# Kernel optimization log

Hardware: AMD Instinct MI355X
Metric: run time of the kernel (lower is better)

The kernel has to match this reference:

```python
import jax, jax.numpy as jnp
import numpy as np

L, D, HQ, HKV, HD, P, V, B, S = 4, 2048, 16, 4, 128, 8192, 32000, 2, 1024
THETA, EPS = 500000.0, 1e-5
RATIO = HQ // HKV  # GQA q-to-kv ratio = 4


def rmsnorm(x, w):
    # torch: w * (x * rsqrt(mean(x^2, -1) + eps)) computed in fp32
    x32 = x.astype(jnp.float32)
    n = x32 * jax.lax.rsqrt(jnp.mean(x32 * x32, axis=-1, keepdims=True) + EPS)
    return w * n.astype(x.dtype)


def make_rope(seq_len):
    inv = 1.0 / (THETA ** (jnp.arange(0, HD, 2, dtype=jnp.float32) / HD))  # [HD/2]
    ang = jnp.arange(seq_len, dtype=jnp.float32)[:, None] * inv[None, :]   # [S, HD/2]
    return jnp.cos(ang)[None, :, None, :], jnp.sin(ang)[None, :, None, :]  # [1,S,1,HD/2]


def rope(t, cos, sin):
    # torch code: complex = t[..., :HD/2] + i*t[..., HD/2:], multiply by e^{i*ang},
    # then view_as_real + flatten -> INTERLEAVED (r0,i0,r1,i1,...) output layout.
    h = HD // 2
    r, im = t[..., :h], t[..., h:]
    orr = r * cos - im * sin
    oim = r * sin + im * cos
    return jnp.stack([orr, oim], axis=-1).reshape(t.shape)


def attention(x, wqkv, wo, cos, sin):
    b, s, _ = x.shape
    qkv = x @ wqkv                               # [b,s,D+2*HKV*HD]
    q = qkv[..., :D].reshape(b, s, HQ, HD)
    k = qkv[..., D:D + HKV * HD].reshape(b, s, HKV, HD)
    v = qkv[..., D + HKV * HD:].reshape(b, s, HKV, HD)
    q = rope(q, cos, sin)
    k = rope(k, cos, sin)
    # GQA: repeat_interleave kv heads to match q heads (offset=0 prefill; cache is identity)
    k = jnp.repeat(k, RATIO, axis=2)
    v = jnp.repeat(v, RATIO, axis=2)
    scale = 1.0 / np.sqrt(HD)
    scores = jnp.einsum('bqhd,bkhd->bhqk', q, k) * scale
    causal = jnp.tril(jnp.ones((s, s), dtype=bool))
    scores = jnp.where(causal[None, None], scores, jnp.finfo(scores.dtype).min)
    probs = jax.nn.softmax(scores, axis=-1)
    out = jnp.einsum('bhqk,bkhd->bqhd', probs, v).reshape(b, s, D)
    return out @ wo


def swiglu(x, wgu, wd):
    gu = x @ wgu                                  # [b,s,2P]
    gate, up = gu[..., :P], gu[..., P:]
    return (jax.nn.silu(gate) * up) @ wd


def setup_inputs() -> dict:
    key = jax.random.key(0)
    ks = jax.random.split(key, 8)
    sc = 0.02
    return {
        'tokens': jax.random.randint(ks[0], (B, S), 0, V),
        'emb': jax.random.normal(ks[1], (V, D), jnp.float32) * sc,
        'w_qkv': jax.random.normal(ks[2], (L, D, D + 2 * HKV * HD), jnp.float32) * sc,
        'w_o': jax.random.normal(ks[3], (L, D, D), jnp.float32) * sc,
        'w_gate_up': jax.random.normal(ks[4], (L, D, 2 * P), jnp.float32) * sc,
        'w_down': jax.random.normal(ks[5], (L, P, D), jnp.float32) * sc,
        'ln_attn': jnp.ones((L, D), jnp.float32),
        'ln_ffn': jnp.ones((L, D), jnp.float32),
        'ln_f': jnp.ones((D,), jnp.float32),
        'w_lm': jax.random.normal(ks[6], (D, V), jnp.float32) * sc,
    }


def reference(tokens, emb, w_qkv, w_o, w_gate_up, w_down, ln_attn, ln_ffn, ln_f, w_lm):
    cos, sin = make_rope(S)
    x = emb[tokens]                               # [B,S,D]
    for l in range(L):
        x = x + attention(rmsnorm(x, ln_attn[l]), w_qkv[l], w_o[l], cos, sin)
        x = x + swiglu(rmsnorm(x, ln_ffn[l]), w_gate_up[l], w_down[l])
    return rmsnorm(x, ln_f) @ w_lm                # logits [B,S,V]
```

## Files before the change

kernel.cpp:

```cpp
#include <hip/hip_runtime.h>
#include <hip/hip_bf16.h>
#include <math.h>

#define S_LEN 1024
#define DIM   2048
#define NHQ   16
#define NHKV  4
#define HDIM  128
#define PDIM  8192
#define VOCAB 32000
#define NLAYER 4
#define NROWS (2 * S_LEN)

typedef __attribute__((ext_vector_type(4))) float f32x4;
typedef __attribute__((ext_vector_type(8))) short bf16x8;

__device__ __forceinline__ void gload_lds16(const void* g, void* l) {
  __builtin_amdgcn_global_load_lds(
      (const __attribute__((address_space(1))) unsigned int*)g,
      (__attribute__((address_space(3))) unsigned int*)l, 16, 0, 0);
}

#define FENCE() asm volatile("" ::: "memory")

__global__ __launch_bounds__(256) void k_embed(const int* __restrict__ tokens,
    const float* __restrict__ emb, float* __restrict__ x) {
  int row = blockIdx.x;
  int tok = tokens[row];
  const f32x4* src = (const f32x4*)(emb + (size_t)tok * DIM);
  f32x4* dst = (f32x4*)(x + (size_t)row * DIM);
  for (int i = threadIdx.x; i < DIM / 4; i += 256) dst[i] = src[i];
}

__global__ __launch_bounds__(256) void k_rmsnorm(const float* __restrict__ x,
    const float* __restrict__ w, __hip_bfloat16* __restrict__ out) {
  int row = blockIdx.x;
  const float* xr = x + (size_t)row * DIM;
  float ss = 0.f;
  for (int i = threadIdx.x; i < DIM; i += 256) { float v = xr[i]; ss += v * v; }
  for (int off = 32; off; off >>= 1) ss += __shfl_xor(ss, off);
  __shared__ float wsum[4];
  if ((threadIdx.x & 63) == 0) wsum[threadIdx.x >> 6] = ss;
  __syncthreads();
  float tot = wsum[0] + wsum[1] + wsum[2] + wsum[3];
  float r = rsqrtf(tot / (float)DIM + 1e-5f);
  __hip_bfloat16* orow = out + (size_t)row * DIM;
  for (int i = threadIdx.x; i < DIM; i += 256)
    orow[i] = __float2bfloat16(w[i] * (xr[i] * r));
}

__global__ __launch_bounds__(256) void k_wt(const float* __restrict__ W,
    __hip_bfloat16* __restrict__ WT, int K, int N) {
  __shared__ __hip_bfloat16 t[64][72];
  int k0 = blockIdx.y * 64, n0 = blockIdx.x * 64;
  int r = threadIdx.x >> 4;
  int c4 = (threadIdx.x & 15) * 4;
#pragma unroll
  for (int i = 0; i < 4; ++i) {
    int k = r + i * 16;
    f32x4 v = *(const f32x4*)(W + (size_t)(k0 + k) * N + n0 + c4);
#pragma unroll
    for (int j = 0; j < 4; ++j) t[c4 + j][k] = __float2bfloat16(v[j]);
  }
  __syncthreads();
  int n = threadIdx.x >> 2, kc = (threadIdx.x & 3) * 16;
  bf16x8* dst = (bf16x8*)(WT + (size_t)(n0 + n) * K + k0 + kc);
  dst[0] = *(const bf16x8*)&t[n][kc];
  dst[1] = *(const bf16x8*)&t[n][kc + 8];
}

template<int EPI>
__global__ __launch_bounds__(512) void k_gemm256(
    const __hip_bfloat16* __restrict__ A, const __hip_bfloat16* __restrict__ BT,
    void* __restrict__ Cv, int M, int N, int K) {
  __shared__ __hip_bfloat16 As[2][256][64];
  __shared__ __hip_bfloat16 Bs[2][256][64];
  int tid = threadIdx.x;
  int bid = blockIdx.x;
  int mt = bid & 7, nt = bid >> 3;
  int bm = mt << 8, bn = nt << 8;
  int wave = tid >> 6, lane = tid & 63;
  int wm = wave >> 2, wn = wave & 3;
  int g = lane >> 4, c = lane & 15;
  f32x4 acc[8][4] = {};

  auto stage = [&](int buf, int k0) {
#pragma unroll
    for (int i = 0; i < 4; ++i) {
      int ci = i * 512 + tid;
      int row = ci >> 3, pc = ci & 7;
      int jl = pc ^ (row & 7);
      gload_lds16(A + (size_t)(bm + row) * K + k0 + jl * 8, &As[buf][row][pc * 8]);
      gload_lds16(BT + (size_t)(bn + row) * K + k0 + jl * 8, &Bs[buf][row][pc * 8]);
    }
  };

  int ntiles = K >> 6;
  stage(0, 0);
  if (ntiles > 1) stage(1, 64);

  for (int t = 0; t < ntiles; ++t) {
    int cur = t & 1;
    if (t + 1 < ntiles) asm volatile("s_waitcnt vmcnt(8)" ::: "memory");
    else                asm volatile("s_waitcnt vmcnt(0)" ::: "memory");
    __builtin_amdgcn_s_barrier();
    FENCE();
    __builtin_amdgcn_sched_barrier(0);
#pragma unroll
    for (int kk = 0; kk < 2; ++kk) {
      bf16x8 af[8], bv[4];
#pragma unroll
      for (int mi = 0; mi < 8; ++mi) {
        int row = wm * 128 + mi * 16 + c;
        int ch = (kk * 4 + g) ^ (row & 7);
        af[mi] = *(const bf16x8*)&As[cur][row][ch * 8];
      }
#pragma unroll
      for (int ni = 0; ni < 4; ++ni) {
        int row = wn * 64 + ni * 16 + c;
        int ch = (kk * 4 + g) ^ (row & 7);
        bv[ni] = *(const bf16x8*)&Bs[cur][row][ch * 8];
      }
      __builtin_amdgcn_s_setprio(1);
#pragma unroll
      for (int mi = 0; mi < 8; ++mi)
#pragma unroll
        for (int ni = 0; ni < 4; ++ni)
          acc[mi][ni] = __builtin_amdgcn_mfma_f32_16x16x32_bf16(af[mi], bv[ni], acc[mi][ni], 0, 0, 0);
      __builtin_amdgcn_s_setprio(0);
    }
    FENCE();
    __builtin_amdgcn_s_barrier();
    FENCE();
    if (t + 2 < ntiles) stage(cur, (t + 2) << 6);
  }

  float* Cf = (float*)Cv;
  __hip_bfloat16* Cb = (__hip_bfloat16*)Cv;
  int row0 = bm + wm * 128, col0 = bn + wn * 64;
#pragma unroll
  for (int mi = 0; mi < 8; ++mi)
#pragma unroll
    for (int ni = 0; ni < 4; ++ni)
#pragma unroll
      for (int r = 0; r < 4; ++r) {
        int row = row0 + mi * 16 + g * 4 + r;
        int col = col0 + ni * 16 + c;
        size_t idx = (size_t)row * N + col;
        if (EPI == 0) Cf[idx] = acc[mi][ni][r];
        else if (EPI == 1) Cf[idx] += acc[mi][ni][r];
        else Cb[idx] = __float2bfloat16(acc[mi][ni][r]);
      }
}

template<int EPI>
__global__ __launch_bounds__(256) void k_gemm_bt(
    const __hip_bfloat16* __restrict__ A, const __hip_bfloat16* __restrict__ BT,
    void* __restrict__ Cv, int M, int N, int K) {
  __shared__ __hip_bfloat16 As[2][128][64];
  __shared__ __hip_bfloat16 Bs[2][128][64];
  int nm = M >> 7;
  int bid = blockIdx.x;
  int mt, nt;
  if (nm == 16) {
    int xcd = bid & 7;
    int seq = bid >> 3;
    mt = (xcd << 1) | (seq & 1);
    nt = seq >> 1;
  } else {
    mt = bid % nm;
    nt = bid / nm;
  }
  int bm = mt << 7, bn = nt << 7;
  int tid  = threadIdx.x;
  int wave = tid >> 6, lane = tid & 63;
  int wr = (wave >> 1) * 64, wc = (wave & 1) * 64;
  int g = lane >> 4, c = lane & 15;
  f32x4 acc[4][4] = {};

  auto stage = [&](int buf, int k0) {
#pragma unroll
    for (int i = 0; i < 4; ++i) {
      int ci = i * 256 + tid;
      int row = ci >> 3, pc = ci & 7;
      int jl = pc ^ (row & 7);
      gload_lds16(A + (size_t)(bm + row) * K + k0 + jl * 8, &As[buf][row][pc * 8]);
      gload_lds16(BT + (size_t)(bn + row) * K + k0 + jl * 8, &Bs[buf][row][pc * 8]);
    }
  };

  int ntiles = K >> 6;
  stage(0, 0);
  if (ntiles > 1) stage(1, 64);

  for (int t = 0; t < ntiles; ++t) {
    int cur = t & 1;
    if (t + 1 < ntiles) asm volatile("s_waitcnt vmcnt(8)" ::: "memory");
    else                asm volatile("s_waitcnt vmcnt(0)" ::: "memory");
    __builtin_amdgcn_s_barrier();
    FENCE();
    __builtin_amdgcn_sched_barrier(0);
#pragma unroll
    for (int kk = 0; kk < 2; ++kk) {
      bf16x8 af[4], bv[4];
#pragma unroll
      for (int mi = 0; mi < 4; ++mi) {
        int row = wr + mi * 16 + c;
        int ch = (kk * 4 + g) ^ (row & 7);
        af[mi] = *(const bf16x8*)&As[cur][row][ch * 8];
      }
#pragma unroll
      for (int ni = 0; ni < 4; ++ni) {
        int row = wc + ni * 16 + c;
        int ch = (kk * 4 + g) ^ (row & 7);
        bv[ni] = *(const bf16x8*)&Bs[cur][row][ch * 8];
      }
      __builtin_amdgcn_s_setprio(1);
#pragma unroll
      for (int mi = 0; mi < 4; ++mi)
#pragma unroll
        for (int ni = 0; ni < 4; ++ni)
          acc[mi][ni] = __builtin_amdgcn_mfma_f32_16x16x32_bf16(af[mi], bv[ni], acc[mi][ni], 0, 0, 0);
      __builtin_amdgcn_s_setprio(0);
    }
    FENCE();
    __builtin_amdgcn_s_barrier();
    FENCE();
    if (t + 2 < ntiles) stage(cur, (t + 2) << 6);
  }

  float* Cf = (float*)Cv;
  __hip_bfloat16* Cb = (__hip_bfloat16*)Cv;
#pragma unroll
  for (int mi = 0; mi < 4; ++mi)
#pragma unroll
    for (int ni = 0; ni < 4; ++ni)
#pragma unroll
      for (int r = 0; r < 4; ++r) {
        int row = bm + wr + mi * 16 + g * 4 + r;
        int col = bn + wc + ni * 16 + c;
        size_t idx = (size_t)row * N + col;
        if (EPI == 0) Cf[idx] = acc[mi][ni][r];
        else if (EPI == 1) Cf[idx] += acc[mi][ni][r];
        else Cb[idx] = __float2bfloat16(acc[mi][ni][r]);
      }
}

template<int EPI>
__global__ __launch_bounds__(256) void k_gemm(
    const __hip_bfloat16* __restrict__ A, const float* __restrict__ Bw,
    void* __restrict__ Cv, int M, int N, int K) {
  __shared__ __hip_bfloat16 As[128][32];
  __shared__ __hip_bfloat16 Bs[128][40];
  int tid  = threadIdx.x;
  int bm = blockIdx.y * 128, bn = blockIdx.x * 128;
  int wave = tid >> 6, lane = tid & 63;
  int wr = (wave >> 1) * 64, wc = (wave & 1) * 64;
  int lrow = lane & 15, lk = (lane >> 4) * 8;
  f32x4 acc[4][4] = {};
  for (int k0 = 0; k0 < K; k0 += 32) {
#pragma unroll
    for (int i = 0; i < 2; ++i) {
      int L = i * 256 + tid;
      int row = L >> 2, koff = (L & 3) * 8;
      gload_lds16(A + (size_t)(bm + row) * K + k0 + koff, &As[row][koff]);
    }
#pragma unroll
    for (int i = 0; i < 4; ++i) {
      int L = i * 256 + tid;
      int kk = L >> 5;
      int c4 = (L & 31) * 4;
      f32x4 v = *(const f32x4*)(Bw + (size_t)(k0 + kk) * N + bn + c4);
#pragma unroll
      for (int j = 0; j < 4; ++j) Bs[c4 + j][kk] = __float2bfloat16(v[j]);
    }
    __syncthreads();
    bf16x8 af[4], bfr[4];
#pragma unroll
    for (int mi = 0; mi < 4; ++mi)
      af[mi] = *(const bf16x8*)(&As[wr + mi * 16 + lrow][lk]);
#pragma unroll
    for (int ni = 0; ni < 4; ++ni)
      bfr[ni] = *(const bf16x8*)(&Bs[wc + ni * 16 + lrow][lk]);
#pragma unroll
    for (int mi = 0; mi < 4; ++mi)
#pragma unroll
      for (int ni = 0; ni < 4; ++ni)
        acc[mi][ni] = __builtin_amdgcn_mfma_f32_16x16x32_bf16(af[mi], bfr[ni], acc[mi][ni], 0, 0, 0);
    __syncthreads();
  }
  float* Cf = (float*)Cv;
  __hip_bfloat16* Cb = (__hip_bfloat16*)Cv;
#pragma unroll
  for (int mi = 0; mi < 4; ++mi)
#pragma unroll
    for (int ni = 0; ni < 4; ++ni)
#pragma unroll
      for (int r = 0; r < 4; ++r) {
        int row = bm + wr + mi * 16 + ((lane >> 4) * 4 + r);
        int col = bn + wc + ni * 16 + (lane & 15);
        size_t idx = (size_t)row * N + col;
        if (EPI == 0) Cf[idx] = acc[mi][ni][r];
        else if (EPI == 1) Cf[idx] += acc[mi][ni][r];
        else Cb[idx] = __float2bfloat16(acc[mi][ni][r]);
      }
}

__global__ __launch_bounds__(256) void k_rope(const float* __restrict__ qkv,
    __hip_bfloat16* __restrict__ qr, __hip_bfloat16* __restrict__ kr,
    __hip_bfloat16* __restrict__ vt) {
  int rowid = blockIdx.x;
  int b = rowid >> 10, s = rowid & (S_LEN - 1);
  const float* src = qkv + (size_t)rowid * 3072;
  const float kInvLog = 0.20503692777f;
  const float scale = 0.08838834764831845f;
  __shared__ float cs[64], sn[64];
  if (threadIdx.x < 64) {
    float inv = expf(-(float)threadIdx.x * kInvLog);
    float a = (float)s * inv;
    sincosf(a, &sn[threadIdx.x], &cs[threadIdx.x]);
  }
  __syncthreads();
  for (int it = threadIdx.x; it < NHQ * 64; it += 256) {
    int h = it >> 6, i = it & 63;
    float re = src[h * HDIM + i], im = src[h * HDIM + 64 + i];
    size_t dst = ((size_t)(b * NHQ + h) * S_LEN + s) * HDIM;
    qr[dst + 2 * i]     = __float2bfloat16((re * cs[i] - im * sn[i]) * scale);
    qr[dst + 2 * i + 1] = __float2bfloat16((re * sn[i] + im * cs[i]) * scale);
  }
  for (int it = threadIdx.x; it < NHKV * 64; it += 256) {
    int h = it >> 6, i = it & 63;
    float re = src[DIM + h * HDIM + i], im = src[DIM + h * HDIM + 64 + i];
    size_t dst = ((size_t)(b * NHKV + h) * S_LEN + s) * HDIM;
    kr[dst + 2 * i]     = __float2bfloat16(re * cs[i] - im * sn[i]);
    kr[dst + 2 * i + 1] = __float2bfloat16(re * sn[i] + im * cs[i]);
  }
  for (int it = threadIdx.x; it < NHKV * HDIM; it += 256) {
    int h = it >> 7, d = it & 127;
    vt[(((size_t)b * NHKV + h) * HDIM + d) * S_LEN + s] =
        __float2bfloat16(src[DIM + NHKV * HDIM + it]);
  }
}

__global__ __launch_bounds__(256) void k_attn_mfma(
    const __hip_bfloat16* __restrict__ Q,
    const __hip_bfloat16* __restrict__ Kc,
    const __hip_bfloat16* __restrict__ VT,
    __hip_bfloat16* __restrict__ O) {
  __shared__ __hip_bfloat16 plds[4][16][40];
  int wave = threadIdx.x >> 6, lane = threadIdx.x & 63;
  int gw = blockIdx.x * 4 + wave;
  int qt = gw & 63;
  int bh = gw >> 6;
  int b = bh >> 4, h = bh & 15;
  int hk = h >> 2;
  int q0 = qt * 16;
  int g = lane >> 4, c = lane & 15;
  const __hip_bfloat16* Qb = Q + ((size_t)bh * S_LEN + q0) * HDIM;
  const __hip_bfloat16* Kb = Kc + (size_t)(b * NHKV + hk) * S_LEN * HDIM;
  const __hip_bfloat16* Vb = VT + (size_t)(b * NHKV + hk) * S_LEN * HDIM;

  bf16x8 qf[4];
#pragma unroll
  for (int cn = 0; cn < 4; ++cn)
    qf[cn] = *(const bf16x8*)(Qb + (size_t)c * HDIM + cn * 32 + g * 8);

  f32x4 po[8] = {};
  float m[4], l[4];
#pragma unroll
  for (int r = 0; r < 4; ++r) { m[r] = -1e30f; l[r] = 0.f; }

  int kvend = q0 + 16;
  for (int kv0 = 0; kv0 < kvend; kv0 += 32) {
    f32x4 s0 = {}, s1 = {};
#pragma unroll
    for (int cn = 0; cn < 4; ++cn) {
      bf16x8 k0f = *(const bf16x8*)(Kb + (size_t)(kv0 + c) * HDIM + cn * 32 + g * 8);
      bf16x8 k1f = *(const bf16x8*)(Kb + (size_t)(kv0 + 16 + c) * HDIM + cn * 32 + g * 8);
      s0 = __builtin_amdgcn_mfma_f32_16x16x32_bf16(qf[cn], k0f, s0, 0, 0, 0);
      s1 = __builtin_amdgcn_mfma_f32_16x16x32_bf16(qf[cn], k1f, s1, 0, 0, 0);
    }
    if (kv0 + 31 > q0) {
#pragma unroll
      for (int r = 0; r < 4; ++r) {
        int qrow = q0 + g * 4 + r;
        if (kv0 + c > qrow)      s0[r] = -1e30f;
        if (kv0 + 16 + c > qrow) s1[r] = -1e30f;
      }
    }
    float rm[4];
#pragma unroll
    for (int r = 0; r < 4; ++r) rm[r] = fmaxf(s0[r], s1[r]);
#pragma unroll
    for (int off = 1; off < 16; off <<= 1)
#pragma unroll
      for (int r = 0; r < 4; ++r) rm[r] = fmaxf(rm[r], __shfl_xor(rm[r], off));
    float p0[4], p1[4], rs[4];
#pragma unroll
    for (int r = 0; r < 4; ++r) {
      float mn = fmaxf(m[r], rm[r]);
      float corr = __expf(m[r] - mn);
      m[r] = mn;
      p0[r] = __expf(s0[r] - mn);
      p1[r] = __expf(s1[r] - mn);
      rs[r] = p0[r] + p1[r];
      l[r] *= corr;
#pragma unroll
      for (int t = 0; t < 8; ++t) po[t][r] *= corr;
    }
#pragma unroll
    for (int off = 1; off < 16; off <<= 1)
#pragma unroll
      for (int r = 0; r < 4; ++r) rs[r] += __shfl_xor(rs[r], off);
#pragma unroll
    for (int r = 0; r < 4; ++r) l[r] += rs[r];
#pragma unroll
    for (int r = 0; r < 4; ++r) {
      plds[wave][g * 4 + r][c]      = __float2bfloat16(p0[r]);
      plds[wave][g * 4 + r][16 + c] = __float2bfloat16(p1[r]);
    }
    bf16x8 pf = *(const bf16x8*)&plds[wave][c][g * 8];
#pragma unroll
    for (int t = 0; t < 8; ++t) {
      bf16x8 vf = *(const bf16x8*)(Vb + (size_t)(t * 16 + c) * S_LEN + kv0 + g * 8);
      po[t] = __builtin_amdgcn_mfma_f32_16x16x32_bf16(pf, vf, po[t], 0, 0, 0);
    }
  }
  float inv[4];
#pragma unroll
  for (int r = 0; r < 4; ++r) inv[r] = 1.f / l[r];
  __hip_bfloat16* ob = O + ((size_t)(b * S_LEN) + q0) * DIM + h * HDIM;
#pragma unroll
  for (int t = 0; t < 8; ++t)
#pragma unroll
    for (int r = 0; r < 4; ++r)
      ob[(size_t)(g * 4 + r) * DIM + t * 16 + c] = __float2bfloat16(po[t][r] * inv[r]);
}

__global__ __launch_bounds__(256) void k_swiglu(const __hip_bfloat16* __restrict__ gu,
    __hip_bfloat16* __restrict__ h) {
  size_t i = (size_t)blockIdx.x * 256 + threadIdx.x;
  size_t row = i >> 10, c8 = (i & 1023) * 8;
  const __hip_bfloat16* grow = gu + row * (2 * PDIM);
  bf16x8 gv = *(const bf16x8*)(grow + c8);
  bf16x8 uv = *(const bf16x8*)(grow + PDIM + c8);
  const __hip_bfloat16* gp = (const __hip_bfloat16*)&gv;
  const __hip_bfloat16* up = (const __hip_bfloat16*)&uv;
  __hip_bfloat16 ov[8];
#pragma unroll
  for (int j = 0; j < 8; ++j) {
    float g = __bfloat162float(gp[j]);
    float u = __bfloat162float(up[j]);
    float s = g / (1.f + __expf(-g));
    ov[j] = __float2bfloat16(s * u);
  }
  *(bf16x8*)(h + row * PDIM + c8) = *(const bf16x8*)ov;
}

extern "C" void kernel_launch(void* const* d_in, const int* in_sizes, int n_in,
                              void* d_out, int out_size, void* d_ws, size_t ws_size,
                              hipStream_t stream) {
  const int*   tokens    = (const int*)d_in[0];
  const float* emb       = (const float*)d_in[1];
  const float* w_qkv     = (const float*)d_in[2];
  const float* w_o       = (const float*)d_in[3];
  const float* w_gate_up = (const float*)d_in[4];
  const float* w_down    = (const float*)d_in[5];
  const float* ln_attn   = (const float*)d_in[6];
  const float* ln_ffn    = (const float*)d_in[7];
  const float* ln_f      = (const float*)d_in[8];
  const float* w_lm      = (const float*)d_in[9];
  float* out = (float*)d_out;

  char* ws = (char*)d_ws;
  float* x = (float*)ws;                    ws += (size_t)NROWS * DIM * 4;
  __hip_bfloat16* xn = (__hip_bfloat16*)ws; ws += (size_t)NROWS * DIM * 2;
  float* qkv = (float*)ws;                  ws += (size_t)NROWS * 3072 * 4;
  __hip_bfloat16* qr = (__hip_bfloat16*)ws; ws += (size_t)2 * NHQ * S_LEN * HDIM * 2;
  __hip_bfloat16* kr = (__hip_bfloat16*)ws; ws += (size_t)2 * NHKV * S_LEN * HDIM * 2;
  __hip_bfloat16* vt = (__hip_bfloat16*)ws; ws += (size_t)2 * NHKV * S_LEN * HDIM * 2;
  __hip_bfloat16* ao = (__hip_bfloat16*)ws; ws += (size_t)NROWS * DIM * 2;
  __hip_bfloat16* gu = (__hip_bfloat16*)ws; ws += (size_t)NROWS * 2 * PDIM * 2;
  __hip_bfloat16* hb = (__hip_bfloat16*)ws; ws += (size_t)NROWS * PDIM * 2;
  __hip_bfloat16* wbuf = (__hip_bfloat16*)ws;
  size_t need = (size_t)(ws - (char*)d_ws) + (size_t)VOCAB * DIM * 2;
  bool bf16w = ws_size >= need;

  k_embed<<<NROWS, 256, 0, stream>>>(tokens, emb, x);

  for (int l = 0; l < NLAYER; ++l) {
    k_rmsnorm<<<NROWS, 256, 0, stream>>>(x, ln_attn + (size_t)l * DIM, xn);
    if (bf16w) {
      k_wt<<<dim3(3072 / 64, DIM / 64), 256, 0, stream>>>(
          w_qkv + (size_t)l * DIM * 3072, wbuf, DIM, 3072);
      k_gemm_bt<0><<<(NROWS / 128) * (3072 / 128), 256, 0, stream>>>(
          xn, wbuf, qkv, NROWS, 3072, DIM);
    } else {
      k_gemm<0><<<dim3(3072 / 128, NROWS / 128), 256, 0, stream>>>(
          xn, w_qkv + (size_t)l * DIM * 3072, qkv, NROWS, 3072, DIM);
    }
    k_rope<<<NROWS, 256, 0, stream>>>(qkv, qr, kr, vt);
    k_attn_mfma<<<(2 * NHQ * (S_LEN / 16)) / 4, 256, 0, stream>>>(qr, kr, vt, ao);
    if (bf16w) {
      k_wt<<<dim3(DIM / 64, DIM / 64), 256, 0, stream>>>(
          w_o + (size_t)l * DIM * DIM, wbuf, DIM, DIM);
      k_gemm_bt<1><<<(NROWS / 128) * (DIM / 128), 256, 0, stream>>>(
          ao, wbuf, x, NROWS, DIM, DIM);
    } else {
      k_gemm<1><<<dim3(DIM / 128, NROWS / 128), 256, 0, stream>>>(
          ao, w_o + (size_t)l * DIM * DIM, x, NROWS, DIM, DIM);
    }
    k_rmsnorm<<<NROWS, 256, 0, stream>>>(x, ln_ffn + (size_t)l * DIM, xn);
    if (bf16w) {
      k_wt<<<dim3(2 * PDIM / 64, DIM / 64), 256, 0, stream>>>(
          w_gate_up + (size_t)l * DIM * 2 * PDIM, wbuf, DIM, 2 * PDIM);
      k_gemm256<2><<<8 * (2 * PDIM / 256), 512, 0, stream>>>(
          xn, wbuf, gu, NROWS, 2 * PDIM, DIM);
    } else {
      k_gemm<2><<<dim3(2 * PDIM / 128, NROWS / 128), 256, 0, stream>>>(
          xn, w_gate_up + (size_t)l * DIM * 2 * PDIM, gu, NROWS, 2 * PDIM, DIM);
    }
    k_swiglu<<<(NROWS * PDIM / 8) / 256, 256, 0, stream>>>(gu, hb);
    if (bf16w) {
      k_wt<<<dim3(DIM / 64, PDIM / 64), 256, 0, stream>>>(
          w_down + (size_t)l * PDIM * DIM, wbuf, PDIM, DIM);
      k_gemm_bt<1><<<(NROWS / 128) * (DIM / 128), 256, 0, stream>>>(
          hb, wbuf, x, NROWS, DIM, PDIM);
    } else {
      k_gemm<1><<<dim3(DIM / 128, NROWS / 128), 256, 0, stream>>>(
          hb, w_down + (size_t)l * PDIM * DIM, x, NROWS, DIM, PDIM);
    }
  }

  k_rmsnorm<<<NROWS, 256, 0, stream>>>(x, ln_f, xn);
  if (bf16w) {
    k_wt<<<dim3(VOCAB / 64, DIM / 64), 256, 0, stream>>>(w_lm, wbuf, DIM, VOCAB);
    k_gemm256<0><<<8 * (VOCAB / 256), 512, 0, stream>>>(
        xn, wbuf, out, NROWS, VOCAB, DIM);
  } else {
    k_gemm<0><<<dim3(VOCAB / 128, NROWS / 128), 256, 0, stream>>>(
        xn, w_lm, out, NROWS, VOCAB, DIM);
  }
}
```

Measured before the change: 2.739 ms.

## Restructure GEMM main loop into four-stage half-K pipeline with new LDS layout

The 256x256 GEMM kernel now streams K in 32-wide slices through a four-deep LDS ring instead of 64-wide slices through a double buffer. Loads for B and A are issued two and three slices ahead, with staggered vmcnt waits. The LDS layout is remapped so each 16-byte chunk lands at a swizzled slot, and fragment reads happen before the next prefetch is issued. The goal is to hide more global-load latency and shorten the time waves sit at barriers. The cost is twice as many barriers per unit of K and fragile hand-counted waitcnt logic.

```diff
diff --git a/kernel.cpp b/kernel.cpp
--- a/kernel.cpp
+++ b/kernel.cpp
@@ -73,8 +73,9 @@
 __global__ __launch_bounds__(512) void k_gemm256(
     const __hip_bfloat16* __restrict__ A, const __hip_bfloat16* __restrict__ BT,
     void* __restrict__ Cv, int M, int N, int K) {
-  __shared__ __hip_bfloat16 As[2][256][64];
-  __shared__ __hip_bfloat16 Bs[2][256][64];
+  __shared__ __hip_bfloat16 AsH[4][128][64];
+  __shared__ __hip_bfloat16 BsH[4][128][64];
+  const int NH = K >> 5;
   int tid = threadIdx.x;
   int bid = blockIdx.x;
   int mt = bid & 7, nt = bid >> 3;
@@ -84,55 +85,66 @@
   int g = lane >> 4, c = lane & 15;
   f32x4 acc[8][4] = {};
 
-  auto stage = [&](int buf, int k0) {
-#pragma unroll
-    for (int i = 0; i < 4; ++i) {
-      int ci = i * 512 + tid;
-      int row = ci >> 3, pc = ci & 7;
-      int jl = pc ^ (row & 7);
-      gload_lds16(A + (size_t)(bm + row) * K + k0 + jl * 8, &As[buf][row][pc * 8]);
-      gload_lds16(BT + (size_t)(bn + row) * K + k0 + jl * 8, &Bs[buf][row][pc * 8]);
+  int pre  = (lane & 7) ^ (lane >> 3);
+  int rOff = (lane >> 3) * 2 + (pre >> 2);
+  int cOff = (pre & 3) * 8;
+
+  auto stageA = [&](int S, int h) {
+#pragma unroll
+    for (int rd = 0; rd < 2; ++rd) {
+      int seg = rd * 8 + wave;
+      gload_lds16(A + (size_t)(bm + seg * 16 + rOff) * K + h * 32 + cOff,
+                  &AsH[S][seg * 8 + (lane >> 3)][(lane & 7) * 8]);
     }
   };
-
-  int ntiles = K >> 6;
-  stage(0, 0);
-  if (ntiles > 1) stage(1, 64);
-
-  for (int t = 0; t < ntiles; ++t) {
-    int cur = t & 1;
-    if (t + 1 < ntiles) asm volatile("s_waitcnt vmcnt(8)" ::: "memory");
-    else                asm volatile("s_waitcnt vmcnt(0)" ::: "memory");
+  auto stageB = [&](int S, int h) {
+#pragma unroll
+    for (int rd = 0; rd < 2; ++rd) {
+      int seg = rd * 8 + wave;
+      gload_lds16(BT + (size_t)(bn + seg * 16 + rOff) * K + h * 32 + cOff,
+                  &BsH[S][seg * 8 + (lane >> 3)][(lane & 7) * 8]);
+    }
+  };
+
+  stageA(0, 0); stageB(0, 0);
+  stageA(1, 1); stageB(1, 1);
+  stageA(2, 2);
+  asm volatile("s_waitcnt vmcnt(6)" ::: "memory");
+  __builtin_amdgcn_s_barrier();
+  FENCE();
+
+  int lineA = wm * 64 + (c >> 1);
+  int lineB = wn * 32 + (c >> 1);
+  int slotE = ((((c & 1) << 2) | g) ^ (c >> 1)) * 8;
+
+  for (int H = 0; H < NH; ++H) {
+    int S = H & 3;
+    bf16x8 af[8], bv[4];
+#pragma unroll
+    for (int mi = 0; mi < 8; ++mi)
+      af[mi] = *(const bf16x8*)&AsH[S][lineA + mi * 8][slotE];
+#pragma unroll
+    for (int ni = 0; ni < 4; ++ni)
+      bv[ni] = *(const bf16x8*)&BsH[S][lineB + ni * 8][slotE];
+    FENCE();
+    if (H + 2 < NH) stageB((H + 2) & 3, H + 2);
+    if (H + 3 < NH) stageA((H + 3) & 3, H + 3);
+    if (H + 4 <= NH)      { asm volatile("s_waitcnt vmcnt(6)" ::: "memory"); }
+    else if (H + 3 == NH) { asm volatile("s_waitcnt vmcnt(4)" ::: "memory"); }
+    else if (H + 2 == NH) { asm volatile("s_waitcnt vmcnt(0)" ::: "memory"); }
     __builtin_amdgcn_s_barrier();
-    FENCE();
+    asm volatile("s_waitcnt lgkmcnt(0)" ::: "memory");
     __builtin_amdgcn_sched_barrier(0);
-#pragma unroll
-    for (int kk = 0; kk < 2; ++kk) {
-      bf16x8 af[8], bv[4];
-#pragma unroll
-      for (int mi = 0; mi < 8; ++mi) {
-        int row = wm * 128 + mi * 16 + c;
-        int ch = (kk * 4 + g) ^ (row & 7);
-        af[mi] = *(const bf16x8*)&As[cur][row][ch * 8];
-      }
-#pragma unroll
-      for (int ni = 0; ni < 4; ++ni) {
-        int row = wn * 64 + ni * 16 + c;
-        int ch = (kk * 4 + g) ^ (row & 7);
-        bv[ni] = *(const bf16x8*)&Bs[cur][row][ch * 8];
-      }
-      __builtin_amdgcn_s_setprio(1);
-#pragma unroll
-      for (int mi = 0; mi < 8; ++mi)
-#pragma unroll
-        for (int ni = 0; ni < 4; ++ni)
-          acc[mi][ni] = __builtin_amdgcn_mfma_f32_16x16x32_bf16(af[mi], bv[ni], acc[mi][ni], 0, 0, 0);
-      __builtin_amdgcn_s_setprio(0);
-    }
+    __builtin_amdgcn_s_setprio(1);
+#pragma unroll
+    for (int mi = 0; mi < 8; ++mi)
+#pragma unroll
+      for (int ni = 0; ni < 4; ++ni)
+        acc[mi][ni] = __builtin_amdgcn_mfma_f32_16x16x32_bf16(af[mi], bv[ni], acc[mi][ni], 0, 0, 0);
+    __builtin_amdgcn_s_setprio(0);
     FENCE();
     __builtin_amdgcn_s_barrier();
     FENCE();
-    if (t + 2 < ntiles) stage(cur, (t + 2) << 6);
   }
 
   float* Cf = (float*)Cv;
```

Measured after the change: 2.697 ms. Within noise of the previous version (-1.5%).
